# Optimization experiments

Hardware: AMD Instinct MI355X
Metric: run time of the kernel (lower is better)

Reference implementation:

```python
import jax, jax.numpy as jnp
import numpy as np

THR = 0.05
BETA = 0.9181805491303656
SLOPE = 13.42287274232855

# straight-through estimator: heaviside fwd, identity bwd
@jax.custom_vjp
def spike_ste(x):
    return (x > 0).astype(x.dtype)
def _ste_fwd(x):
    return (x > 0).astype(x.dtype), None
def _ste_bwd(res, g):
    return (g,)
spike_ste.defvjp(_ste_fwd, _ste_bwd)

# fast sigmoid surrogate: heaviside fwd, grad 1/(slope*|x|+1)^2 bwd
@jax.custom_vjp
def spike_fs(x):
    return (x > 0).astype(x.dtype)
def _fs_fwd(x):
    return (x > 0).astype(x.dtype), x
def _fs_bwd(x, g):
    return (g / (SLOPE * jnp.abs(x) + 1.0) ** 2,)
spike_fs.defvjp(_fs_fwd, _fs_bwd)

def _conv(x, w, b):
    y = jax.lax.conv_general_dilated(x, w, (1, 1), 'SAME', dimension_numbers=('NCHW', 'OIHW', 'NCHW'))
    return y + b[None, :, None, None]

def _maxpool2(x):
    return jax.lax.reduce_window(x, -jnp.inf, jax.lax.max, (1, 1, 2, 2), (1, 1, 2, 2), 'VALID')

def _sconvlstm(x, syn, mem, w, b):
    # snntorch SConvLSTM: conv over cat(input, hidden) -> 4 gates; reset_mechanism='none'
    gates = _conv(jnp.concatenate([x, mem], axis=1), w, b)
    cc_i, cc_f, cc_g, cc_o = jnp.split(gates, 4, axis=1)
    syn = jax.nn.sigmoid(cc_f) * syn + jax.nn.sigmoid(cc_i) * jnp.tanh(cc_g)
    mem = jax.nn.sigmoid(cc_o) * jnp.tanh(syn)
    spk = spike_ste(_maxpool2(mem) - THR)  # spike on max-pooled membrane
    return spk, syn, mem

def _leaky(cur, mem):
    # snntorch Leaky, reset_mechanism='subtract'; reset computed from previous mem, detached
    reset = jax.lax.stop_gradient((mem > THR).astype(mem.dtype))
    mem = BETA * mem + cur - reset * THR
    spk = spike_fs(mem - THR)
    return spk, mem

def setup_inputs():
    key = jax.random.key(0)
    ks = jax.random.split(key, 11)
    T, B, H, W = 25, 64, 16, 128
    x = jax.random.normal(ks[0], (T, B, H, W), jnp.float32)
    def cw(k, o, i):
        return jax.random.normal(k, (o, i, 3, 3), jnp.float32) / np.float32(np.sqrt(i * 9))
    w1 = cw(ks[1], 64, 17)
    b1 = jax.random.normal(ks[2], (64,), jnp.float32) * 0.01
    w2 = cw(ks[3], 128, 48)
    b2 = jax.random.normal(ks[4], (128,), jnp.float32) * 0.01
    w3 = cw(ks[5], 256, 96)
    b3 = jax.random.normal(ks[6], (256,), jnp.float32) * 0.01
    fc1_w = jax.random.normal(ks[7], (512, 2048), jnp.float32) / np.float32(np.sqrt(2048))
    fc1_b = jax.random.normal(ks[8], (512,), jnp.float32) * 0.01
    fc2_w = jax.random.normal(ks[9], (2, 512), jnp.float32) / np.float32(np.sqrt(512))
    fc2_b = jax.random.normal(ks[10], (2,), jnp.float32) * 0.01
    return dict(x=x, w1=w1, b1=b1, w2=w2, b2=b2, w3=w3, b3=b3,
                fc1_w=fc1_w, fc1_b=fc1_b, fc2_w=fc2_w, fc2_b=fc2_b)

def reference(x, w1, b1, w2, b2, w3, b3, fc1_w, fc1_b, fc2_w, fc2_b):
    T, B, H, W = x.shape
    z = lambda c, h, w: jnp.zeros((B, c, h, w), x.dtype)
    carry = (z(16, H, W), z(16, H, W),
             z(32, H // 2, W // 2), z(32, H // 2, W // 2),
             z(64, H // 4, W // 4), z(64, H // 4, W // 4),
             jnp.zeros((B, 512), x.dtype), jnp.zeros((B, 2), x.dtype))
    def step(carry, xt):
        syn1, mem1, syn2, mem2, syn3, mem3, mem4, mem5 = carry
        spk1, syn1, mem1 = _sconvlstm(xt[:, None], syn1, mem1, w1, b1)
        spk2, syn2, mem2 = _sconvlstm(spk1, syn2, mem2, w2, b2)
        spk3, syn3, mem3 = _sconvlstm(spk2, syn3, mem3, w3, b3)
        cur4 = spk3.reshape(B, -1) @ fc1_w.T + fc1_b  # dropout = identity (eval mode)
        spk4, mem4 = _leaky(cur4, mem4)
        cur5 = spk4 @ fc2_w.T + fc2_b
        spk5, mem5 = _leaky(cur5, mem5)
        return (syn1, mem1, syn2, mem2, syn3, mem3, mem4, mem5), (spk5, mem5)
    _, (spk_rec, mem_rec) = jax.lax.scan(step, carry, x)
    return spk_rec, mem_rec
```

## Files before the change

### kernel.cpp

```cpp
#include <hip/hip_runtime.h>
#include <math.h>
#include <stdint.h>

#define THR  0.05f
#define BETA 0.9181805491303656f
#define B_SZ 64
#define T_STEPS 25

using h8    = __attribute__((ext_vector_type(8))) _Float16;
using f32x4 = __attribute__((ext_vector_type(4))) float;

__device__ __forceinline__ float sigf(float x) { return 1.0f / (1.0f + __expf(-x)); }
__device__ __forceinline__ float tanh_fast(float x) {
    const float xc = fminf(fmaxf(x, -10.0f), 10.0f);
    const float e = __expf(2.0f * xc);
    return (e - 1.0f) / (e + 1.0f);
}

__global__ __launch_bounds__(256) void repack_kernel(
    const float* __restrict__ wt, float* __restrict__ wr, int Ch, int CIN)
{
    const int n = 4 * Ch * CIN * 9;
    for (int i = blockIdx.x * 256 + threadIdx.x; i < n; i += gridDim.x * 256) {
        const int g   = i & 3;
        const int tap = (i >> 2) % 9;
        const int ci  = (i / 36) % CIN;
        const int c   = i / (36 * CIN);
        wr[i] = wt[(((size_t)(g * Ch + c)) * CIN + ci) * 9 + tap];
    }
}

__global__ __launch_bounds__(256) void repack_mfma_kernel(
    const float* __restrict__ wt, _Float16* __restrict__ whi, _Float16* __restrict__ wlo,
    int Ch, int CIN, int KS)
{
    const int NG = (4 * Ch) / 16;
    const int n = 9 * KS * NG * 512;
    for (int i = blockIdx.x * 256 + threadIdx.x; i < n; i += gridDim.x * 256) {
        const int j   = i & 7;
        const int l   = (i >> 3) & 63;
        const int ng  = (i >> 9) % NG;
        const int ks  = (i / (512 * NG)) % KS;
        const int tap = i / (512 * NG * KS);
        const int o   = ng * 16 + (l & 15);
        const int ci  = ks * 32 + ((l >> 4) << 3) + j;
        const float w = (ci < CIN) ? wt[((size_t)o * CIN + ci) * 9 + tap] : 0.0f;
        const _Float16 hi = (_Float16)w;
        whi[i] = hi;
        wlo[i] = (_Float16)(w - (float)hi);
    }
}

template<int CSPK, int Ch, int H, int W, int H_T, int KS, int CIN_S, bool POOL>
__global__ __launch_bounds__(256) void convlstm_mfma(
    const float* __restrict__ xin,
    const float* __restrict__ memin,
    const float* __restrict__ synin,
    float* __restrict__ synout,
    float* __restrict__ memout,
    const _Float16* __restrict__ whi,
    const _Float16* __restrict__ wlo,
    const float* __restrict__ bias)
{
    constexpr int CIN   = CSPK + Ch;
    constexpr int W2    = W + 2;
    constexpr int ROWS  = (H_T + 2) * W2;
    constexpr int NELEM = ROWS * CIN_S + 16;
    constexpr int NCG   = Ch / 16;
    constexpr int MSPLIT = H / H_T;
    constexpr int M_T   = H_T * W;
    constexpr int WM    = M_T / 4;
    constexpr int MF    = WM / 16;
    constexpr int NG    = (4 * Ch) / 16;
    constexpr int SPAIRS = W / 2;
    constexpr int NCP   = CIN / 2;
    static_assert(WM % 16 == 0 && W % 16 == 0, "");
    static_assert(KS * 32 <= CIN_S + 16, "last k-read must stay inside NELEM slack");
    static_assert(CIN_S >= CIN, "channels must fit the padded stride");
    static_assert(CIN % 2 == 0 && CSPK % 2 == 0 && CIN_S % 2 == 0, "pair packing");

    __shared__ _Float16 tileH[NELEM];
    __shared__ _Float16 tileL[NELEM];

    const int tid = threadIdx.x;
    const int bid = blockIdx.x;
    const int cg = bid % NCG;
    const int ms = (bid / NCG) % MSPLIT;
    const int b  = bid / (NCG * MSPLIT);
    const int y0 = ms * H_T;
    const int c0 = cg * 16;

    {
        uint32_t* p0 = (uint32_t*)tileH;
        uint32_t* p1 = (uint32_t*)tileL;
        for (int i = tid; i < NELEM / 2; i += 256) { p0[i] = 0u; p1[i] = 0u; }
    }
    __syncthreads();

    for (int i = tid; i < NCP * (H_T + 2) * SPAIRS; i += 256) {
        const int px = i % SPAIRS;
        const int ry = (i / SPAIRS) % (H_T + 2);
        const int cp = i / (SPAIRS * (H_T + 2));
        const int ci = 2 * cp;
        const int y  = y0 + ry - 1;
        if (y < 0 || y >= H) continue;
        const int x0 = 2 * px;
        float v[2][2];
        #pragma unroll
        for (int d = 0; d < 2; ++d) {
            const int c = ci + d;
            if (POOL && c < CSPK) {
                const float* mp = xin + (((size_t)b * CSPK + c) * (2 * H) + 2 * y) * (2 * W) + 2 * x0;
                const float4 q0 = *(const float4*)mp;
                const float4 q1 = *(const float4*)(mp + 2 * W);
                v[d][0] = ((fmaxf(fmaxf(q0.x, q0.y), fmaxf(q1.x, q1.y)) - THR) > 0.0f) ? 1.0f : 0.0f;
                v[d][1] = ((fmaxf(fmaxf(q0.z, q0.w), fmaxf(q1.z, q1.w)) - THR) > 0.0f) ? 1.0f : 0.0f;
            } else if (c < CSPK) {
                const float2 q = *(const float2*)(xin + (((size_t)b * CSPK + c) * H + y) * W + x0);
                v[d][0] = q.x; v[d][1] = q.y;
            } else {
                const float2 q = *(const float2*)(memin + (((size_t)b * Ch + (c - CSPK)) * H + y) * W + x0);
                v[d][0] = q.x; v[d][1] = q.y;
            }
        }
        #pragma unroll
        for (int dx = 0; dx < 2; ++dx) {
            const int off = (ry * W2 + x0 + dx + 1) * CIN_S + ci;
            const _Float16 h0 = (_Float16)v[0][dx];
            const _Float16 h1 = (_Float16)v[1][dx];
            const _Float16 l0 = (_Float16)(v[0][dx] - (float)h0);
            const _Float16 l1 = (_Float16)(v[1][dx] - (float)h1);
            const uint32_t ph = (uint32_t)__builtin_bit_cast(uint16_t, h0)
                              | ((uint32_t)__builtin_bit_cast(uint16_t, h1) << 16);
            const uint32_t pl = (uint32_t)__builtin_bit_cast(uint16_t, l0)
                              | ((uint32_t)__builtin_bit_cast(uint16_t, l1) << 16);
            *(uint32_t*)(tileH + off) = ph;
            *(uint32_t*)(tileL + off) = pl;
        }
    }
    __syncthreads();

    const int lane = tid & 63;
    const int wid  = tid >> 6;
    const int l15  = lane & 15;
    const int lk8  = (lane >> 4) << 3;

    f32x4 acc[MF][4];
    #pragma unroll
    for (int g = 0; g < 4; ++g) {
        const float bb = bias[g * Ch + c0 + l15];
        #pragma unroll
        for (int m = 0; m < MF; ++m) acc[m][g] = f32x4{bb, bb, bb, bb};
    }

    #pragma unroll 3
    for (int tap = 0; tap < 9; ++tap) {
        const int dy = tap / 3, dx = tap % 3;
        #pragma unroll
        for (int ks = 0; ks < KS; ++ks) {
            h8 bh[4], bl[4];
            #pragma unroll
            for (int g = 0; g < 4; ++g) {
                const size_t base = ((((size_t)tap * KS + ks) * NG + g * NCG + cg) * 64 + lane) * 8;
                bh[g] = *(const h8*)(whi + base);
                bl[g] = *(const h8*)(wlo + base);
            }
            #pragma unroll
            for (int m = 0; m < MF; ++m) {
                const int pxf = wid * WM + m * 16;
                const int yl = pxf / W;
                const int xf = pxf % W;
                const int off = ((yl + dy) * W2 + xf + l15 + dx) * CIN_S + ks * 32 + lk8;
                const h8 ah = *(const h8*)(tileH + off);
                const h8 al = *(const h8*)(tileL + off);
                #pragma unroll
                for (int g = 0; g < 4; ++g) {
                    acc[m][g] = __builtin_amdgcn_mfma_f32_16x16x32_f16(ah, bh[g], acc[m][g], 0, 0, 0);
                    acc[m][g] = __builtin_amdgcn_mfma_f32_16x16x32_f16(ah, bl[g], acc[m][g], 0, 0, 0);
                    acc[m][g] = __builtin_amdgcn_mfma_f32_16x16x32_f16(al, bh[g], acc[m][g], 0, 0, 0);
                }
            }
        }
    }

    #pragma unroll
    for (int m = 0; m < MF; ++m) {
        const int pxf = wid * WM + m * 16;
        const int yl = pxf / W;
        const int xf = pxf % W;
        const int c = c0 + l15;
        #pragma unroll
        for (int j = 0; j < 4; ++j) {
            const int x = xf + ((lane >> 4) << 2) + j;
            const size_t gaddr = (((size_t)b * Ch + c) * H + (y0 + yl)) * W + x;
            const float gi = acc[m][0][j], gf = acc[m][1][j];
            const float gg = acc[m][2][j], go = acc[m][3][j];
            const float syn = sigf(gf) * synin[gaddr] + sigf(gi) * tanh_fast(gg);
            synout[gaddr] = syn;
            memout[gaddr] = sigf(go) * tanh_fast(syn);
        }
    }
}

template<int Cin, int Ch, int H, int W, int R, int CSPLIT, int CHUNK,
         bool POOL_IN, int MINW, int P, int UF>
__global__ __launch_bounds__(256, MINW) void conv_lstm(
    const float* __restrict__ xin,
    const float* __restrict__ memin,
    const float* __restrict__ synin,
    float* __restrict__ synout,
    float* __restrict__ memout,
    const float* __restrict__ wr,
    const float* __restrict__ bias)
{
    constexpr int CIN = Cin + Ch;
    constexpr int R2 = R + 2;
    constexpr int SW = W + 4;
    constexpr int ROWLANES = W / P;
    constexpr int SPAIRS = W / 2;
    constexpr int NROUNDS = CIN / CHUNK;
    constexpr int CITERS = Ch / (CSPLIT * 4);
    constexpr int PRE = CHUNK % UF;
    static_assert(R * ROWLANES == 64, "");
    static_assert(CIN % CHUNK == 0, "");

    __shared__ float tile[CHUNK * R2 * SW];

    const int tid = threadIdx.x;
    const int bid = blockIdx.x;
    const int cs = bid % CSPLIT;
    const int rs = (bid / CSPLIT) % (H / R);
    const int b  = bid / (CSPLIT * (H / R));
    const int r0 = rs * R;
    const int c0 = cs * (Ch / CSPLIT);

    const int lane = tid & 63;
    const int wid  = tid >> 6;
    const int ly   = lane / ROWLANES;
    const int lx   = P * (lane % ROWLANES);
    const int gy_out = r0 + ly;

    int cu[CITERS];
    #pragma unroll
    for (int k = 0; k < CITERS; ++k)
        cu[k] = __builtin_amdgcn_readfirstlane(c0 + k * 4 + wid);

    float acc[CITERS][4 * P];
    #pragma unroll
    for (int k = 0; k < CITERS; ++k) {
        const float bi = bias[cu[k]];
        const float bf = bias[cu[k] + Ch];
        const float bg = bias[cu[k] + 2 * Ch];
        const float bo = bias[cu[k] + 3 * Ch];
        #pragma unroll
        for (int p = 0; p < P; ++p) {
            acc[k][0 * P + p] = bi;
            acc[k][1 * P + p] = bf;
            acc[k][2 * P + p] = bg;
            acc[k][3 * P + p] = bo;
        }
    }

    for (int rd = 0; rd < NROUNDS; ++rd) {
        const int k0 = rd * CHUNK;
        if (rd) __syncthreads();

        for (int i = tid; i < CHUNK * R2 * 4; i += 256) {
            const int col = i & 3;
            const int row = i >> 2;
            tile[row * SW + (col == 0 ? 0 : W + col)] = 0.0f;
        }
        for (int i = tid; i < CHUNK * R2 * SPAIRS; i += 256) {
            const int px  = i % SPAIRS;
            const int ry  = (i / SPAIRS) % R2;
            const int cil = i / (SPAIRS * R2);
            const int ci  = k0 + cil;
            const int gy  = r0 + ry - 1;
            float vx = 0.0f, vy = 0.0f;
            if (gy >= 0 && gy < H) {
                if (POOL_IN && ci < Cin) {
                    const float* mp = xin + (((size_t)b * Cin + ci) * (2 * H) + 2 * gy) * (2 * W) + 4 * px;
                    const float4 q0 = *(const float4*)mp;
                    const float4 q1 = *(const float4*)(mp + 2 * W);
                    vx = ((fmaxf(fmaxf(q0.x, q0.y), fmaxf(q1.x, q1.y)) - THR) > 0.0f) ? 1.0f : 0.0f;
                    vy = ((fmaxf(fmaxf(q0.z, q0.w), fmaxf(q1.z, q1.w)) - THR) > 0.0f) ? 1.0f : 0.0f;
                } else if (ci < Cin) {
                    const float2 q = *(const float2*)(xin + (((size_t)b * Cin + ci) * H + gy) * W + 2 * px);
                    vx = q.x; vy = q.y;
                } else {
                    const float2 q = *(const float2*)(memin + (((size_t)b * Ch + (ci - Cin)) * H + gy) * W + 2 * px);
                    vx = q.x; vy = q.y;
                }
            }
            const int t0 = (cil * R2 + ry) * SW + 1 + 2 * px;
            tile[t0]     = vx;
            tile[t0 + 1] = vy;
        }
        __syncthreads();

        auto body = [&](int cil) {
            float s[3][P + 2];
            #pragma unroll
            for (int dy = 0; dy < 3; ++dy) {
                const float* rp = &tile[(cil * R2 + ly + dy) * SW + lx];
                if constexpr (P == 4) {
                    const float4 a  = *(const float4*)rp;
                    const float2 e  = *(const float2*)(rp + 4);
                    s[dy][0] = a.x; s[dy][1] = a.y; s[dy][2] = a.z; s[dy][3] = a.w;
                    s[dy][4] = e.x; s[dy][5] = e.y;
                } else {
                    const float2 a  = *(const float2*)rp;
                    const float2 e  = *(const float2*)(rp + 2);
                    s[dy][0] = a.x; s[dy][1] = a.y; s[dy][2] = e.x; s[dy][3] = e.y;
                }
            }
            #pragma unroll
            for (int k = 0; k < CITERS; ++k) {
                const float* wp = wr + ((size_t)cu[k] * CIN + (k0 + cil)) * 36;
                #pragma unroll
                for (int tap = 0; tap < 9; ++tap) {
                    const int dy = tap / 3, dx = tap % 3;
                    const float wi  = wp[tap * 4 + 0];
                    const float wf  = wp[tap * 4 + 1];
                    const float wg_ = wp[tap * 4 + 2];
                    const float wo  = wp[tap * 4 + 3];
                    #pragma unroll
                    for (int p = 0; p < P; ++p) {
                        const float v = s[dy][p + dx];
                        acc[k][0 * P + p] = fmaf(v, wi,  acc[k][0 * P + p]);
                        acc[k][1 * P + p] = fmaf(v, wf,  acc[k][1 * P + p]);
                        acc[k][2 * P + p] = fmaf(v, wg_, acc[k][2 * P + p]);
                        acc[k][3 * P + p] = fmaf(v, wo,  acc[k][3 * P + p]);
                    }
                }
            }
        };

        #pragma unroll
        for (int cil = 0; cil < PRE; ++cil) body(cil);
        #pragma unroll 1
        for (int cil0 = PRE; cil0 < CHUNK; cil0 += UF) {
            #pragma unroll
            for (int u = 0; u < UF; ++u) body(cil0 + u);
        }
    }

    #pragma unroll
    for (int k = 0; k < CITERS; ++k) {
        const int c = c0 + k * 4 + wid;
        const size_t base = (((size_t)b * Ch + c) * H + gy_out) * W + lx;
        float sv[P], so[P], mo[P];
        if constexpr (P == 4) {
            const float4 q = *(const float4*)(synin + base);
            sv[0] = q.x; sv[1] = q.y; sv[2] = q.z; sv[3] = q.w;
        } else {
            const float2 q = *(const float2*)(synin + base);
            sv[0] = q.x; sv[1] = q.y;
        }
        #pragma unroll
        for (int p = 0; p < P; ++p) {
            const float syn = sigf(acc[k][1 * P + p]) * sv[p]
                            + sigf(acc[k][0 * P + p]) * tanh_fast(acc[k][2 * P + p]);
            so[p] = syn;
            mo[p] = sigf(acc[k][3 * P + p]) * tanh_fast(syn);
        }
        if constexpr (P == 4) {
            *(float4*)(synout + base) = make_float4(so[0], so[1], so[2], so[3]);
            *(float4*)(memout + base) = make_float4(mo[0], mo[1], mo[2], mo[3]);
        } else {
            *(float2*)(synout + base) = make_float2(so[0], so[1]);
            *(float2*)(memout + base) = make_float2(mo[0], mo[1]);
        }
    }
}

__global__ __launch_bounds__(256) void fc1_pool_kernel(
    const float* __restrict__ m3,
    const float* __restrict__ wt,
    const float* __restrict__ bias,
    float* __restrict__ mem4,
    float* __restrict__ spk4)
{
    const int wid = (blockIdx.x * 256 + threadIdx.x) >> 6;
    const int lane = threadIdx.x & 63;
    const int og = wid & 63;
    const int b = wid >> 6;
    const int o0 = og * 8;

    float acc[8] = {0, 0, 0, 0, 0, 0, 0, 0};
    for (int it = 0; it < 8; ++it) {
        const int k = (it * 64 + lane) * 4;
        const int c = k >> 5;
        const int rem = k & 31;
        const int ph = rem >> 4;
        const int pw = rem & 15;
        const float* mp = m3 + (((size_t)b * 64 + c) * 4 + 2 * ph) * 32 + 2 * pw;
        const float4 r0 = *(const float4*)mp;
        const float4 r1 = *(const float4*)(mp + 4);
        const float4 q0 = *(const float4*)(mp + 32);
        const float4 q1 = *(const float4*)(mp + 36);
        float4 sv;
        sv.x = ((fmaxf(fmaxf(r0.x, r0.y), fmaxf(q0.x, q0.y)) - THR) > 0.0f) ? 1.0f : 0.0f;
        sv.y = ((fmaxf(fmaxf(r0.z, r0.w), fmaxf(q0.z, q0.w)) - THR) > 0.0f) ? 1.0f : 0.0f;
        sv.z = ((fmaxf(fmaxf(r1.x, r1.y), fmaxf(q1.x, q1.y)) - THR) > 0.0f) ? 1.0f : 0.0f;
        sv.w = ((fmaxf(fmaxf(r1.z, r1.w), fmaxf(q1.z, q1.w)) - THR) > 0.0f) ? 1.0f : 0.0f;
        #pragma unroll
        for (int j = 0; j < 8; ++j) {
            const float4 wv = *(const float4*)(wt + (size_t)(o0 + j) * 2048 + k);
            acc[j] = fmaf(sv.x, wv.x, acc[j]);
            acc[j] = fmaf(sv.y, wv.y, acc[j]);
            acc[j] = fmaf(sv.z, wv.z, acc[j]);
            acc[j] = fmaf(sv.w, wv.w, acc[j]);
        }
    }
    float mine = 0.0f;
    #pragma unroll
    for (int j = 0; j < 8; ++j) {
        float a = acc[j];
        #pragma unroll
        for (int off = 32; off; off >>= 1) a += __shfl_xor(a, off, 64);
        if (lane == j) mine = a;
    }
    if (lane < 8) {
        const int o = o0 + lane;
        const float cur = mine + bias[o];
        const int i4 = b * 512 + o;
        float m = mem4[i4];
        const float reset = (m > THR) ? 1.0f : 0.0f;
        m = BETA * m + cur - reset * THR;
        spk4[i4] = ((m - THR) > 0.0f) ? 1.0f : 0.0f;
        mem4[i4] = m;
    }
}

__global__ __launch_bounds__(256) void fc2_kernel(
    const float* __restrict__ spk4,
    const float* __restrict__ wt,
    const float* __restrict__ bias,
    float* __restrict__ mem5,
    float* __restrict__ out_spk,
    float* __restrict__ out_mem)
{
    const int wid = (blockIdx.x * 256 + threadIdx.x) >> 6;
    const int lane = threadIdx.x & 63;
    if (wid >= 2 * B_SZ) return;
    const int o = wid & 1;
    const int b = wid >> 1;
    const float* wr = wt + (size_t)o * 512;
    const float* sr = spk4 + (size_t)b * 512;
    float acc = 0.0f;
    #pragma unroll
    for (int i = 0; i < 8; ++i)
        acc = fmaf(sr[lane + i * 64], wr[lane + i * 64], acc);
    #pragma unroll
    for (int off = 32; off; off >>= 1) acc += __shfl_down(acc, off, 64);
    if (lane == 0) {
        const float cur = acc + bias[o];
        const int i5 = b * 2 + o;
        float m = mem5[i5];
        const float reset = (m > THR) ? 1.0f : 0.0f;
        m = BETA * m + cur - reset * THR;
        out_spk[i5] = ((m - THR) > 0.0f) ? 1.0f : 0.0f;
        out_mem[i5] = m;
        mem5[i5] = m;
    }
}

extern "C" void kernel_launch(void* const* d_in, const int* in_sizes, int n_in,
                              void* d_out, int out_size, void* d_ws, size_t ws_size,
                              hipStream_t stream) {
    (void)in_sizes; (void)n_in; (void)out_size; (void)ws_size;

    const float* x    = (const float*)d_in[0];
    const float* w1   = (const float*)d_in[1];
    const float* b1   = (const float*)d_in[2];
    const float* w2   = (const float*)d_in[3];
    const float* b2   = (const float*)d_in[4];
    const float* w3   = (const float*)d_in[5];
    const float* b3   = (const float*)d_in[6];
    const float* fc1w = (const float*)d_in[7];
    const float* fc1b = (const float*)d_in[8];
    const float* fc2w = (const float*)d_in[9];
    const float* fc2b = (const float*)d_in[10];

    float* out = (float*)d_out;
    float* ws = (float*)d_ws;

    const size_t N1 = (size_t)B_SZ * 16 * 16 * 128;
    const size_t N2 = (size_t)B_SZ * 32 * 8 * 64;
    const size_t N3 = (size_t)B_SZ * 64 * 4 * 32;

    size_t off = 0;
    float* syn1  = ws + off; off += N1;
    float* mem1a = ws + off; off += N1;
    float* syn2  = ws + off; off += N2;
    float* mem2a = ws + off; off += N2;
    float* syn3  = ws + off; off += N3;
    float* mem3a = ws + off; off += N3;
    float* mem4  = ws + off; off += (size_t)B_SZ * 512;
    float* mem5  = ws + off; off += (size_t)B_SZ * 2;
    const size_t zero_elems = off;
    float* mem1b = ws + off; off += N1;
    float* mem2b = ws + off; off += N2;
    float* mem3b = ws + off; off += N3;
    float* spk4  = ws + off; off += (size_t)B_SZ * 512;
    float* wr1   = ws + off; off += (size_t)4 * 16 * 17 * 9;
    _Float16* whi2 = (_Float16*)(ws + off); off += 36864;
    _Float16* wlo2 = (_Float16*)(ws + off); off += 36864;
    _Float16* whi3 = (_Float16*)(ws + off); off += 110592;
    _Float16* wlo3 = (_Float16*)(ws + off); off += 110592;

    (void)hipMemsetAsync(d_ws, 0, zero_elems * sizeof(float), stream);

    repack_kernel<<<64, 256, 0, stream>>>(w1, wr1, 16, 17);
    repack_mfma_kernel<<<288, 256, 0, stream>>>(w2, whi2, wlo2, 32, 48, 2);
    repack_mfma_kernel<<<864, 256, 0, stream>>>(w3, whi3, wlo3, 64, 96, 3);

    float* m1r = mem1a; float* m1w = mem1b;
    float* m2r = mem2a; float* m2w = mem2b;
    float* m3r = mem3a; float* m3w = mem3b;

    for (int t = 0; t < T_STEPS; ++t) {
        const float* xt = x + (size_t)t * B_SZ * 16 * 128;

        conv_lstm<1, 16, 16, 128, 2, 2, 17, false, 4, 4, 4><<<1024, 256, 0, stream>>>(
            xt, m1r, syn1, syn1, m1w, wr1, b1);

        convlstm_mfma<16, 32, 8, 64, 2, 2, 56, true><<<512, 256, 0, stream>>>(
            m1w, m2r, syn2, syn2, m2w, whi2, wlo2, b2);

        convlstm_mfma<32, 64, 4, 32, 2, 3, 104, true><<<512, 256, 0, stream>>>(
            m2w, m3r, syn3, syn3, m3w, whi3, wlo3, b3);

        fc1_pool_kernel<<<1024, 256, 0, stream>>>(m3w, fc1w, fc1b, mem4, spk4);
        fc2_kernel<<<32, 256, 0, stream>>>(
            spk4, fc2w, fc2b, mem5, out + (size_t)t * 2 * B_SZ,
            out + 3200 + (size_t)t * 2 * B_SZ);

        float* tmp;
        tmp = m1r; m1r = m1w; m1w = tmp;
        tmp = m2r; m2r = m2w; m2w = tmp;
        tmp = m3r; m3r = m3w; m3w = tmp;
    }
}
```

Measured before the change: 2.926 ms.

## Use 512-thread blocks covering all channels in first ConvLSTM layer

Makes the block size of the scalar conv_lstm kernel a template parameter. Layer 1 now launches 512-thread blocks with CSPLIT=1, so each block covers all 16 hidden channels and the staged input tile is loaded once per row pair instead of twice. The tile fill now moves four floats per thread with float4 loads, and the manual UF unroll of the channel loop is replaced by a plain non-unrolled loop. The risks are lower occupancy from larger blocks, less instruction-level parallelism in the inner loop, and fewer blocks in the grid.

After: 2.781 ms. 5.0% less time.

```diff
diff --git a/kernel.cpp b/kernel.cpp
--- a/kernel.cpp
+++ b/kernel.cpp
@@ -203,8 +203,8 @@
 }
 
 template<int Cin, int Ch, int H, int W, int R, int CSPLIT, int CHUNK,
-         bool POOL_IN, int MINW, int P, int UF>
-__global__ __launch_bounds__(256, MINW) void conv_lstm(
+         bool POOL_IN, int MINW, int P, int NT>
+__global__ __launch_bounds__(NT, MINW) void conv_lstm(
     const float* __restrict__ xin,
     const float* __restrict__ memin,
     const float* __restrict__ synin,
@@ -217,12 +217,13 @@
     constexpr int R2 = R + 2;
     constexpr int SW = W + 4;
     constexpr int ROWLANES = W / P;
-    constexpr int SPAIRS = W / 2;
+    constexpr int SQ = W / 4;
     constexpr int NROUNDS = CIN / CHUNK;
-    constexpr int CITERS = Ch / (CSPLIT * 4);
-    constexpr int PRE = CHUNK % UF;
+    constexpr int NW = NT / 64;
+    constexpr int CITERS = Ch / (CSPLIT * NW);
     static_assert(R * ROWLANES == 64, "");
     static_assert(CIN % CHUNK == 0, "");
+    static_assert(W % 4 == 0, "");
 
     __shared__ float tile[CHUNK * R2 * SW];
 
@@ -243,7 +244,7 @@
     int cu[CITERS];
     #pragma unroll
     for (int k = 0; k < CITERS; ++k)
-        cu[k] = __builtin_amdgcn_readfirstlane(c0 + k * 4 + wid);
+        cu[k] = __builtin_amdgcn_readfirstlane(c0 + k * NW + wid);
 
     float acc[CITERS][4 * P];
     #pragma unroll
@@ -265,40 +266,47 @@
         const int k0 = rd * CHUNK;
         if (rd) __syncthreads();
 
-        for (int i = tid; i < CHUNK * R2 * 4; i += 256) {
+        for (int i = tid; i < CHUNK * R2 * 4; i += NT) {
             const int col = i & 3;
             const int row = i >> 2;
             tile[row * SW + (col == 0 ? 0 : W + col)] = 0.0f;
         }
-        for (int i = tid; i < CHUNK * R2 * SPAIRS; i += 256) {
-            const int px  = i % SPAIRS;
-            const int ry  = (i / SPAIRS) % R2;
-            const int cil = i / (SPAIRS * R2);
+        for (int i = tid; i < CHUNK * R2 * SQ; i += NT) {
+            const int q   = i % SQ;
+            const int ry  = (i / SQ) % R2;
+            const int cil = i / (SQ * R2);
             const int ci  = k0 + cil;
             const int gy  = r0 + ry - 1;
-            float vx = 0.0f, vy = 0.0f;
+            float v0 = 0.0f, v1 = 0.0f, v2 = 0.0f, v3 = 0.0f;
             if (gy >= 0 && gy < H) {
                 if (POOL_IN && ci < Cin) {
-                    const float* mp = xin + (((size_t)b * Cin + ci) * (2 * H) + 2 * gy) * (2 * W) + 4 * px;
-                    const float4 q0 = *(const float4*)mp;
-                    const float4 q1 = *(const float4*)(mp + 2 * W);
-                    vx = ((fmaxf(fmaxf(q0.x, q0.y), fmaxf(q1.x, q1.y)) - THR) > 0.0f) ? 1.0f : 0.0f;
-                    vy = ((fmaxf(fmaxf(q0.z, q0.w), fmaxf(q1.z, q1.w)) - THR) > 0.0f) ? 1.0f : 0.0f;
+                    const float* mp = xin + (((size_t)b * Cin + ci) * (2 * H) + 2 * gy) * (2 * W) + 8 * q;
+                    const float4 a0 = *(const float4*)mp;
+                    const float4 a1 = *(const float4*)(mp + 4);
+                    const float4 b0 = *(const float4*)(mp + 2 * W);
+                    const float4 b1 = *(const float4*)(mp + 2 * W + 4);
+                    v0 = ((fmaxf(fmaxf(a0.x, a0.y), fmaxf(b0.x, b0.y)) - THR) > 0.0f) ? 1.0f : 0.0f;
+                    v1 = ((fmaxf(fmaxf(a0.z, a0.w), fmaxf(b0.z, b0.w)) - THR) > 0.0f) ? 1.0f : 0.0f;
+                    v2 = ((fmaxf(fmaxf(a1.x, a1.y), fmaxf(b1.x, b1.y)) - THR) > 0.0f) ? 1.0f : 0.0f;
+                    v3 = ((fmaxf(fmaxf(a1.z, a1.w), fmaxf(b1.z, b1.w)) - THR) > 0.0f) ? 1.0f : 0.0f;
                 } else if (ci < Cin) {
-                    const float2 q = *(const float2*)(xin + (((size_t)b * Cin + ci) * H + gy) * W + 2 * px);
-                    vx = q.x; vy = q.y;
+                    const float4 a = *(const float4*)(xin + (((size_t)b * Cin + ci) * H + gy) * W + 4 * q);
+                    v0 = a.x; v1 = a.y; v2 = a.z; v3 = a.w;
                 } else {
-                    const float2 q = *(const float2*)(memin + (((size_t)b * Ch + (ci - Cin)) * H + gy) * W + 2 * px);
-                    vx = q.x; vy = q.y;
+                    const float4 a = *(const float4*)(memin + (((size_t)b * Ch + (ci - Cin)) * H + gy) * W + 4 * q);
+                    v0 = a.x; v1 = a.y; v2 = a.z; v3 = a.w;
                 }
             }
-            const int t0 = (cil * R2 + ry) * SW + 1 + 2 * px;
-            tile[t0]     = vx;
-            tile[t0 + 1] = vy;
+            const int t0 = (cil * R2 + ry) * SW + 1 + 4 * q;
+            tile[t0]     = v0;
+            tile[t0 + 1] = v1;
+            tile[t0 + 2] = v2;
+            tile[t0 + 3] = v3;
         }
         __syncthreads();
 
-        auto body = [&](int cil) {
+        #pragma unroll 1
+        for (int cil = 0; cil < CHUNK; ++cil) {
             float s[3][P + 2];
             #pragma unroll
             for (int dy = 0; dy < 3; ++dy) {
@@ -334,20 +342,12 @@
                     }
                 }
             }
-        };
-
-        #pragma unroll
-        for (int cil = 0; cil < PRE; ++cil) body(cil);
-        #pragma unroll 1
-        for (int cil0 = PRE; cil0 < CHUNK; cil0 += UF) {
-            #pragma unroll
-            for (int u = 0; u < UF; ++u) body(cil0 + u);
         }
     }
 
     #pragma unroll
     for (int k = 0; k < CITERS; ++k) {
-        const int c = c0 + k * 4 + wid;
+        const int c = c0 + k * NW + wid;
         const size_t base = (((size_t)b * Ch + c) * H + gy_out) * W + lx;
         float sv[P], so[P], mo[P];
         if constexpr (P == 4) {
@@ -523,7 +523,7 @@
     for (int t = 0; t < T_STEPS; ++t) {
         const float* xt = x + (size_t)t * B_SZ * 16 * 128;
 
-        conv_lstm<1, 16, 16, 128, 2, 2, 17, false, 4, 4, 4><<<1024, 256, 0, stream>>>(
+        conv_lstm<1, 16, 16, 128, 2, 1, 17, false, 4, 4, 512><<<512, 512, 0, stream>>>(
             xt, m1r, syn1, syn1, m1w, wr1, b1);
 
         convlstm_mfma<16, 32, 8, 64, 2, 2, 56, true><<<512, 256, 0, stream>>>(
```
